# Optimization experiments

Measured on AMD Instinct MI355X. Metric: run time of the kernel, lower is better.

Reference implementation:

```python
import jax, jax.numpy as jnp
import numpy as np

TOP_K = 8
NUM_GROUPS = 8


def setup_inputs() -> dict:
    key = jax.random.key(0)
    ks = jax.random.split(key, 6)
    T_B, T_S, H, I, E, G = 1, 2048, 2048, 768, 32, NUM_GROUPS
    hidden_states = jax.random.normal(ks[0], (T_B, T_S, H), dtype=jnp.float32)
    gate_weight = jax.random.normal(ks[1], (E, H), dtype=jnp.float32) * 0.02
    gate_up_proj = jax.random.normal(ks[2], (E, 2 * I, H), dtype=jnp.float32) * 0.02
    down_proj = jax.random.normal(ks[3], (E, H, I), dtype=jnp.float32) * 0.02
    merge_groups = jax.random.randint(ks[4], (E,), 0, G, dtype=jnp.int64)
    # ensure every group id appears at least once so dominant experts are well-defined
    merge_groups = merge_groups.at[:G].set(jnp.arange(G, dtype=jnp.int64))
    dominant_experts = jax.random.randint(ks[5], (G,), 0, E, dtype=jnp.int64)
    return {
        "hidden_states": hidden_states,
        "gate_weight": gate_weight,
        "gate_up_proj": gate_up_proj,
        "down_proj": down_proj,
        "merge_groups": merge_groups,
        "dominant_experts": dominant_experts,
    }


def reference(hidden_states, gate_weight, gate_up_proj, down_proj, merge_groups, dominant_experts):
    B, S, H = hidden_states.shape
    G = dominant_experts.shape[0]
    x = hidden_states.reshape(-1, H)  # [T, H]

    # Router: softmax over all experts, then top-k of the probabilities (as in source)
    logits = jnp.einsum("th,eh->te", x, gate_weight)
    probs = jax.nn.softmax(logits.astype(jnp.float32), axis=-1).astype(logits.dtype)
    top_val, top_idx = jax.lax.top_k(probs, TOP_K)  # [T, K]
    top_val = top_val / jnp.sum(top_val, axis=-1, keepdims=True)  # norm_topk_prob

    # Each selected expert e is replaced by its group's dominant expert; by linearity
    # of the scatter-add combine, sum routing weights per (token, group).
    sel_group = merge_groups[top_idx]  # [T, K] in [0, G)
    onehot = jax.nn.one_hot(sel_group, G, dtype=top_val.dtype)  # [T, K, G]
    w_tg = jnp.einsum("tk,tkg->tg", top_val, onehot)  # combined weight per token/group

    gu = gate_up_proj[dominant_experts]  # [G, 2I, H]
    dn = down_proj[dominant_experts]     # [G, H, I]

    h = jnp.einsum("th,goh->tgo", x, gu)           # [T, G, 2I]
    gate, up = jnp.split(h, 2, axis=-1)              # [T, G, I] each
    act = jax.nn.silu(gate) * up                     # SwiGLU
    y = jnp.einsum("tgi,ghi->tgh", act, dn)        # [T, G, H]
    out = jnp.einsum("tg,tgh->th", w_tg, y)        # combine
    return out.reshape(B, S, H)
```

## Files before the change

kernel.cpp:

```cpp
#include <hip/hip_runtime.h>
#include <hip/hip_bf16.h>

typedef __attribute__((ext_vector_type(8))) short short8v;
typedef __attribute__((ext_vector_type(4))) float f32x4;

#define T_TOK 2048
#define HDIM  2048
#define IDIM  768
#define NGRP  8

__device__ __forceinline__ unsigned short f2b(float f){
  unsigned u = __float_as_uint(f);
  u = u + 0x7FFFu + ((u >> 16) & 1u);
  return (unsigned short)(u >> 16);
}
__device__ __forceinline__ float b2f(unsigned short s){
  return __uint_as_float(((unsigned)s) << 16);
}

__global__ __launch_bounds__(256) void router_kernel(
    const float* __restrict__ x, const float* __restrict__ gw,
    const int* __restrict__ mg, float* __restrict__ wtg,
    unsigned short* __restrict__ xb)
{
  __shared__ float xs[4][2048];
  __shared__ float lg[4][32];
  int tid = threadIdx.x;
  int t0 = blockIdx.x * 4;

  #pragma unroll
  for (int k = 0; k < 8; k++){
    int idx = k*256 + tid;
    int tok = idx >> 9, wi = idx & 511;
    float4 v = ((const float4*)(x + (size_t)(t0 + tok)*HDIM))[wi];
    ((float4*)xs[tok])[wi] = v;
    ushort4 b; b.x=f2b(v.x); b.y=f2b(v.y); b.z=f2b(v.z); b.w=f2b(v.w);
    ((ushort4*)(xb + (size_t)(t0+tok)*HDIM))[wi] = b;
  }
  __syncthreads();

  int e = tid >> 3, ch = tid & 7;
  float s0=0.f, s1=0.f, s2=0.f, s3=0.f;
  const float4* gv = (const float4*)(gw + (size_t)e*HDIM);
  #pragma unroll 4
  for (int k = 0; k < 64; k++){
    int i4 = ch + 8*k;
    float4 b  = gv[i4];
    float4 a0 = ((const float4*)xs[0])[i4];
    float4 a1 = ((const float4*)xs[1])[i4];
    float4 a2 = ((const float4*)xs[2])[i4];
    float4 a3 = ((const float4*)xs[3])[i4];
    s0 += a0.x*b.x + a0.y*b.y + a0.z*b.z + a0.w*b.w;
    s1 += a1.x*b.x + a1.y*b.y + a1.z*b.z + a1.w*b.w;
    s2 += a2.x*b.x + a2.y*b.y + a2.z*b.z + a2.w*b.w;
    s3 += a3.x*b.x + a3.y*b.y + a3.z*b.z + a3.w*b.w;
  }
  #pragma unroll
  for (int off=1; off<8; off<<=1){
    s0 += __shfl_xor(s0, off); s1 += __shfl_xor(s1, off);
    s2 += __shfl_xor(s2, off); s3 += __shfl_xor(s3, off);
  }
  if (ch == 0){ lg[0][e]=s0; lg[1][e]=s1; lg[2][e]=s2; lg[3][e]=s3; }
  __syncthreads();

  int wv = tid >> 6, lane = tid & 63;
  float val = (lane < 32) ? lg[wv][lane] : -1e30f;
  float mx = val;
  #pragma unroll
  for (int off=16; off; off>>=1) mx = fmaxf(mx, __shfl_xor(mx, off));
  float p = (lane < 32) ? expf(val - mx) : 0.f;
  float sm = p;
  #pragma unroll
  for (int off=16; off; off>>=1) sm += __shfl_xor(sm, off);
  float v = (lane < 32) ? (p / sm) : -1.f;
  int idx = lane;
  float vals[8]; int idxs[8];
  #pragma unroll
  for (int it=0; it<8; it++){
    float bv = v; int bi = idx;
    #pragma unroll
    for (int off=32; off; off>>=1){
      float ov = __shfl_xor(bv, off); int oi = __shfl_xor(bi, off);
      if (ov > bv || (ov == bv && oi < bi)){ bv = ov; bi = oi; }
    }
    vals[it] = bv; idxs[it] = bi;
    if (lane == bi) v = -1.f;
  }
  float tot = vals[0]+vals[1]+vals[2]+vals[3]+vals[4]+vals[5]+vals[6]+vals[7];
  float racc = 0.f;
  #pragma unroll
  for (int it=0; it<8; it++){
    int grp = mg[idxs[it]];
    if (lane == grp) racc += vals[it] / tot;
  }
  if (lane < 8) wtg[(size_t)(t0+wv)*NGRP + lane] = racc;
}

__global__ __launch_bounds__(256) void convert_gu_kernel(
    const float* __restrict__ src, unsigned short* __restrict__ dst,
    const int* __restrict__ de)
{
  int g = blockIdx.z;
  int i4 = blockIdx.x*256 + threadIdx.x;
  int j  = i4 >> 9;
  int c4 = i4 & 511;
  int q = j >> 5, r = j & 31;
  int srow = (r < 16) ? (q*16 + r) : (768 + q*16 + (r - 16));
  const float4* s = (const float4*)(src + ((size_t)de[g]*1536 + srow)*HDIM);
  float4 vv = s[c4];
  ushort4 b; b.x=f2b(vv.x); b.y=f2b(vv.y); b.z=f2b(vv.z); b.w=f2b(vv.w);
  ((ushort4*)(dst + ((size_t)g*1536 + j)*HDIM))[c4] = b;
}

__global__ __launch_bounds__(256) void convert_dn_kernel(
    const float* __restrict__ src, unsigned short* __restrict__ dst,
    const int* __restrict__ de)
{
  int g = blockIdx.z;
  size_t i4 = (size_t)blockIdx.x*256 + threadIdx.x;
  const float4* s = (const float4*)(src + (size_t)de[g]*1572864);
  float4 vv = s[i4];
  ushort4 b; b.x=f2b(vv.x); b.y=f2b(vv.y); b.z=f2b(vv.z); b.w=f2b(vv.w);
  ((ushort4*)(dst + (size_t)g*1572864))[i4] = b;
}


template<int R>
__device__ __forceinline__ void stage_tile(const unsigned short* __restrict__ gsrc,
                                           int ldE, unsigned short* __restrict__ lds,
                                           int tid)
{
  #pragma unroll
  for (int j = 0; j < R/128; j++){
    int row = j*128 + (tid >> 2);
    const unsigned short* src = gsrc + (size_t)row*ldE + (tid & 3)*8;
    __builtin_amdgcn_global_load_lds(
        (const __attribute__((address_space(1))) void*)src,
        (__attribute__((address_space(3))) void*)(lds + j*4096 + (tid >> 6)*512),
        16, 0, 0);
  }
}

__device__ __forceinline__ short8v rfrag(const unsigned short* lds, int r, int s){
  return *(const short8v*)((const char*)lds + r*64 + (s << 4));
}

#define WAITV(N)  asm volatile("s_waitcnt vmcnt(" #N ")" ::: "memory")
#define TOPBAR()  do { __builtin_amdgcn_s_barrier(); __builtin_amdgcn_sched_barrier(0); } while(0)

__global__ __launch_bounds__(512, 2) void gemm1_kernel(
    const unsigned short* __restrict__ xb, const unsigned short* __restrict__ gu,
    const float* __restrict__ wtg, unsigned short* __restrict__ actb)
{
  __shared__ unsigned short Al[4][8192];
  __shared__ unsigned short Bl[4][4096];
  int tid = threadIdx.x, lane = tid & 63, w = tid >> 6;
  int wm = w >> 1, wn = w & 1;
  int fr = lane & 15, sl = lane >> 4;

  int bid = blockIdx.x;
  int xcd = bid & 7, j = bid >> 3;
  int panel = ((xcd & 1) ? 48 : 0) + (j >> 1);
  int mb = ((xcd >> 1) << 1) + (j & 1);
  int nb = panel % 12, g = panel / 12;
  int m0 = mb * 256, n0 = nb * 128;
  const unsigned short* Abase = xb + (size_t)m0 * HDIM;
  const unsigned short* Bbase = gu + ((size_t)g * 1536 + n0) * HDIM;

  f32x4 acc[4][4];
  #pragma unroll
  for (int m=0;m<4;m++){
    #pragma unroll
    for (int n=0;n<4;n++) acc[m][n] = (f32x4){0,0,0,0};
  }

  #define BODY1(t, DOSTAGE) do { \
    int buf = (t) & 3; \
    short8v av[4], bv[4]; \
    _Pragma("unroll") for (int m=0;m<4;m++) av[m] = rfrag(&Al[buf][0], wm*64 + m*16 + fr, sl); \
    _Pragma("unroll") for (int n=0;n<4;n++) bv[n] = rfrag(&Bl[buf][0], wn*64 + n*16 + fr, sl); \
    if (DOSTAGE){ int k2 = (t)+3, b2 = k2 & 3; \
      stage_tile<256>(Abase + k2*32, HDIM, &Al[b2][0], tid); \
      stage_tile<128>(Bbase + k2*32, HDIM, &Bl[b2][0], tid); } \
    _Pragma("unroll") for (int m=0;m<4;m++){ \
      _Pragma("unroll") for (int n=0;n<4;n++){ \
        acc[m][n] = __builtin_amdgcn_mfma_f32_16x16x32_bf16(av[m], bv[n], acc[m][n],0,0,0); } } \
  } while(0)

  const int NT = 64;
  stage_tile<256>(Abase,      HDIM, &Al[0][0], tid); stage_tile<128>(Bbase,      HDIM, &Bl[0][0], tid);
  stage_tile<256>(Abase + 32, HDIM, &Al[1][0], tid); stage_tile<128>(Bbase + 32, HDIM, &Bl[1][0], tid);
  stage_tile<256>(Abase + 64, HDIM, &Al[2][0], tid); stage_tile<128>(Bbase + 64, HDIM, &Bl[2][0], tid);

  for (int t = 0; t < NT-3; ++t){
    WAITV(6); TOPBAR();
    BODY1(t, 1);
  }
  WAITV(6); TOPBAR(); BODY1(NT-3, 0);
  WAITV(3); TOPBAR(); BODY1(NT-2, 0);
  WAITV(0); TOPBAR(); BODY1(NT-1, 0);
  #undef BODY1

  int r0 = (lane >> 4) * 4;
  int q0 = (n0 + wn*64) >> 5;
  #pragma unroll
  for (int m = 0; m < 4; m++){
    int trow = m0 + wm*64 + m*16 + r0;
    #pragma unroll
    for (int q = 0; q < 2; q++){
      int icol = (q0 + q)*16 + fr;
      #pragma unroll
      for (int jj = 0; jj < 4; jj++){
        int t = trow + jj;
        float wv = wtg[(size_t)t*NGRP + g];
        float gf = acc[m][2*q][jj];
        float uf = acc[m][2*q+1][jj];
        float sg = gf / (1.f + expf(-gf));
        actb[((size_t)g*T_TOK + t)*IDIM + icol] = f2b(sg * uf * wv);
      }
    }
  }
}

__global__ __launch_bounds__(512, 2) void gemm2_kernel(
    const unsigned short* __restrict__ actb, const unsigned short* __restrict__ dnb,
    float* __restrict__ part)
{
  __shared__ unsigned short Al[4][4096];
  __shared__ unsigned short Bl[4][8192];
  int tid = threadIdx.x, lane = tid & 63, w = tid >> 6;
  int wm = w >> 2, wn = w & 3;
  int fr = lane & 15, sl = lane >> 4;

  int bid = blockIdx.x;
  int xcd = bid & 7, j = bid >> 3;
  int panel = ((xcd & 1) ? 8 : 0) + (j >> 2);
  int mb = ((xcd >> 1) << 2) + (j & 3);
  int nb = panel & 7, z = panel >> 3;
  int m0 = mb * 128, n0 = nb * 256;

  f32x4 acc[4][4];
  #pragma unroll
  for (int m=0;m<4;m++){
    #pragma unroll
    for (int n=0;n<4;n++) acc[m][n] = (f32x4){0,0,0,0};
  }

  #define STAGE2(kt, b2) do { \
    int gi = (kt) / 24; int kk = ((kt) - gi*24) * 32; int gg = z*4 + gi; \
    stage_tile<128>(actb + ((size_t)gg*T_TOK + m0)*IDIM + kk, IDIM, &Al[b2][0], tid); \
    stage_tile<256>(dnb  + ((size_t)gg*HDIM + n0)*IDIM + kk, IDIM, &Bl[b2][0], tid); \
  } while(0)

  #define BODY2(t, DOSTAGE) do { \
    int buf = (t) & 3; \
    short8v av[4], bv[4]; \
    _Pragma("unroll") for (int m=0;m<4;m++) av[m] = rfrag(&Al[buf][0], wm*64 + m*16 + fr, sl); \
    _Pragma("unroll") for (int n=0;n<4;n++) bv[n] = rfrag(&Bl[buf][0], wn*64 + n*16 + fr, sl); \
    if (DOSTAGE){ int k2 = (t)+3; STAGE2(k2, k2 & 3); } \
    _Pragma("unroll") for (int m=0;m<4;m++){ \
      _Pragma("unroll") for (int n=0;n<4;n++){ \
        acc[m][n] = __builtin_amdgcn_mfma_f32_16x16x32_bf16(av[m], bv[n], acc[m][n],0,0,0); } } \
  } while(0)

  const int NT = 96;
  STAGE2(0, 0); STAGE2(1, 1); STAGE2(2, 2);

  for (int t = 0; t < NT-3; ++t){
    WAITV(6); TOPBAR();
    BODY2(t, 1);
  }
  WAITV(6); TOPBAR(); BODY2(NT-3, 0);
  WAITV(3); TOPBAR(); BODY2(NT-2, 0);
  WAITV(0); TOPBAR(); BODY2(NT-1, 0);
  #undef BODY2
  #undef STAGE2

  float* Cb = part + (size_t)z * T_TOK * HDIM;
  int r0 = (lane >> 4) * 4;
  #pragma unroll
  for (int m = 0; m < 4; m++){
    int row = m0 + wm*64 + m*16 + r0;
    #pragma unroll
    for (int n = 0; n < 4; n++){
      int cc = n0 + wn*64 + n*16 + fr;
      #pragma unroll
      for (int jj = 0; jj < 4; jj++){
        Cb[(size_t)(row + jj)*HDIM + cc] = acc[m][n][jj];
      }
    }
  }
}

__global__ __launch_bounds__(256) void reduce_kernel(
    const float* __restrict__ p, float* __restrict__ o)
{
  size_t i = ((size_t)blockIdx.x*256 + threadIdx.x)*4;
  float4 a0 = *(const float4*)(p + i);
  float4 a1 = *(const float4*)(p + 4194304 + i);
  float4 r;
  r.x = a0.x + a1.x;
  r.y = a0.y + a1.y;
  r.z = a0.z + a1.z;
  r.w = a0.w + a1.w;
  *(float4*)(o + i) = r;
}

extern "C" void kernel_launch(void* const* d_in, const int* in_sizes, int n_in,
                              void* d_out, int out_size, void* d_ws, size_t ws_size,
                              hipStream_t stream)
{
  (void)in_sizes; (void)n_in; (void)out_size; (void)ws_size;
  const float* x   = (const float*)d_in[0];
  const float* gw  = (const float*)d_in[1];
  const float* gup = (const float*)d_in[2];
  const float* dnp = (const float*)d_in[3];
  const int*   mg  = (const int*)d_in[4];
  const int*   de  = (const int*)d_in[5];
  float* out = (float*)d_out;
  char* ws = (char*)d_ws;

  float*          wtg  = (float*)(ws + 0);
  unsigned short* xb   = (unsigned short*)(ws + 65536);
  unsigned short* dnb  = (unsigned short*)(ws + 8454144);
  unsigned short* actb = (unsigned short*)(ws + 33619968);
  unsigned short* gub  = (unsigned short*)(ws + 58785792);
  float*          part = (float*)(ws + 58785792);

  router_kernel<<<512, 256, 0, stream>>>(x, gw, mg, wtg, xb);
  convert_gu_kernel<<<dim3(3072,1,8), 256, 0, stream>>>(gup, gub, de);
  convert_dn_kernel<<<dim3(1536,1,8), 256, 0, stream>>>(dnp, dnb, de);
  gemm1_kernel<<<768, 512, 0, stream>>>(xb, gub, wtg, actb);
  gemm2_kernel<<<256, 512, 0, stream>>>(actb, dnb, part);
  reduce_kernel<<<4096, 256, 0, stream>>>(part, out);
}
```

Measured before the change: 253.9 us.

## Enlarge per-wave GEMM tiles, triple-buffer LDS, and split down-proj K four ways

gemm1 now runs 4 waves per block instead of 8, and each wave computes a 128x64 tile. This doubles MFMA work per LDS fragment load and shrinks the LDS ring to three stages with a prefetch distance of two. gemm2 moves to 256x256 tiles with K split four ways (two groups per split) instead of two, using the same triple-buffer scheme. Both GEMMs also wait on LDS reads before the MFMA block and raise wave priority around it. The reduce kernel now sums four fp32 partials, which adds extra global memory traffic, and the larger accumulator arrays raise register pressure.

```diff
diff --git a/kernel.cpp b/kernel.cpp
--- a/kernel.cpp
+++ b/kernel.cpp
@@ -126,9 +126,9 @@
 
 
 template<int R>
-__device__ __forceinline__ void stage_tile(const unsigned short* __restrict__ gsrc,
-                                           int ldE, unsigned short* __restrict__ lds,
-                                           int tid)
+__device__ __forceinline__ void stage512(const unsigned short* __restrict__ gsrc,
+                                         int ldE, unsigned short* __restrict__ lds,
+                                         int tid)
 {
   #pragma unroll
   for (int j = 0; j < R/128; j++){
@@ -141,19 +141,36 @@
   }
 }
 
+template<int R>
+__device__ __forceinline__ void stage256(const unsigned short* __restrict__ gsrc,
+                                         int ldE, unsigned short* __restrict__ lds,
+                                         int tid)
+{
+  #pragma unroll
+  for (int j = 0; j < R/64; j++){
+    int row = j*64 + (tid >> 2);
+    const unsigned short* src = gsrc + (size_t)row*ldE + (tid & 3)*8;
+    __builtin_amdgcn_global_load_lds(
+        (const __attribute__((address_space(1))) void*)src,
+        (__attribute__((address_space(3))) void*)(lds + j*2048 + (tid >> 6)*512),
+        16, 0, 0);
+  }
+}
+
 __device__ __forceinline__ short8v rfrag(const unsigned short* lds, int r, int s){
   return *(const short8v*)((const char*)lds + r*64 + (s << 4));
 }
 
 #define WAITV(N)  asm volatile("s_waitcnt vmcnt(" #N ")" ::: "memory")
 #define TOPBAR()  do { __builtin_amdgcn_s_barrier(); __builtin_amdgcn_sched_barrier(0); } while(0)
-
-__global__ __launch_bounds__(512, 2) void gemm1_kernel(
+#define PIN()     do { asm volatile("s_waitcnt lgkmcnt(0)" ::: "memory"); __builtin_amdgcn_sched_barrier(0); } while(0)
+
+__global__ __launch_bounds__(256, 2) void gemm1_kernel(
     const unsigned short* __restrict__ xb, const unsigned short* __restrict__ gu,
     const float* __restrict__ wtg, unsigned short* __restrict__ actb)
 {
-  __shared__ unsigned short Al[4][8192];
-  __shared__ unsigned short Bl[4][4096];
+  __shared__ unsigned short Al[3][8192];
+  __shared__ unsigned short Bl[3][4096];
   int tid = threadIdx.x, lane = tid & 63, w = tid >> 6;
   int wm = w >> 1, wn = w & 1;
   int fr = lane & 15, sl = lane >> 4;
@@ -167,45 +184,52 @@
   const unsigned short* Abase = xb + (size_t)m0 * HDIM;
   const unsigned short* Bbase = gu + ((size_t)g * 1536 + n0) * HDIM;
 
-  f32x4 acc[4][4];
-  #pragma unroll
-  for (int m=0;m<4;m++){
+  f32x4 acc[8][4];
+  #pragma unroll
+  for (int m=0;m<8;m++){
     #pragma unroll
     for (int n=0;n<4;n++) acc[m][n] = (f32x4){0,0,0,0};
   }
 
-  #define BODY1(t, DOSTAGE) do { \
-    int buf = (t) & 3; \
-    short8v av[4], bv[4]; \
-    _Pragma("unroll") for (int m=0;m<4;m++) av[m] = rfrag(&Al[buf][0], wm*64 + m*16 + fr, sl); \
-    _Pragma("unroll") for (int n=0;n<4;n++) bv[n] = rfrag(&Bl[buf][0], wn*64 + n*16 + fr, sl); \
-    if (DOSTAGE){ int k2 = (t)+3, b2 = k2 & 3; \
-      stage_tile<256>(Abase + k2*32, HDIM, &Al[b2][0], tid); \
-      stage_tile<128>(Bbase + k2*32, HDIM, &Bl[b2][0], tid); } \
-    _Pragma("unroll") for (int m=0;m<4;m++){ \
+  #define BODY1(t, CB, SB, DOSTAGE) do { \
+    const unsigned short* Ab = &Al[CB][0]; \
+    const unsigned short* Bb = &Bl[CB][0]; \
+    short8v av[8], bv[4]; \
+    _Pragma("unroll") for (int m=0;m<8;m++) av[m] = rfrag(Ab, wm*128 + m*16 + fr, sl); \
+    _Pragma("unroll") for (int n=0;n<4;n++) bv[n] = rfrag(Bb, wn*64 + n*16 + fr, sl); \
+    if (DOSTAGE){ int k2 = (t)+2; \
+      stage256<256>(Abase + k2*32, HDIM, &Al[SB][0], tid); \
+      stage256<128>(Bbase + k2*32, HDIM, &Bl[SB][0], tid); } \
+    PIN(); \
+    __builtin_amdgcn_s_setprio(1); \
+    _Pragma("unroll") for (int m=0;m<8;m++){ \
       _Pragma("unroll") for (int n=0;n<4;n++){ \
         acc[m][n] = __builtin_amdgcn_mfma_f32_16x16x32_bf16(av[m], bv[n], acc[m][n],0,0,0); } } \
+    __builtin_amdgcn_s_setprio(0); \
   } while(0)
 
   const int NT = 64;
-  stage_tile<256>(Abase,      HDIM, &Al[0][0], tid); stage_tile<128>(Bbase,      HDIM, &Bl[0][0], tid);
-  stage_tile<256>(Abase + 32, HDIM, &Al[1][0], tid); stage_tile<128>(Bbase + 32, HDIM, &Bl[1][0], tid);
-  stage_tile<256>(Abase + 64, HDIM, &Al[2][0], tid); stage_tile<128>(Bbase + 64, HDIM, &Bl[2][0], tid);
-
-  for (int t = 0; t < NT-3; ++t){
+  stage256<256>(Abase,      HDIM, &Al[0][0], tid);
+  stage256<128>(Bbase,      HDIM, &Bl[0][0], tid);
+  stage256<256>(Abase + 32, HDIM, &Al[1][0], tid);
+  stage256<128>(Bbase + 32, HDIM, &Bl[1][0], tid);
+
+  int cb = 0, sb = 2;
+  for (int t = 0; t < NT-2; ++t){
     WAITV(6); TOPBAR();
-    BODY1(t, 1);
-  }
-  WAITV(6); TOPBAR(); BODY1(NT-3, 0);
-  WAITV(3); TOPBAR(); BODY1(NT-2, 0);
-  WAITV(0); TOPBAR(); BODY1(NT-1, 0);
+    BODY1(t, cb, sb, 1);
+    cb = (cb==2)?0:cb+1; sb = (sb==2)?0:sb+1;
+  }
+  WAITV(6); TOPBAR(); BODY1(NT-2, cb, sb, 0);
+  cb = (cb==2)?0:cb+1;
+  WAITV(0); TOPBAR(); BODY1(NT-1, cb, sb, 0);
   #undef BODY1
 
   int r0 = (lane >> 4) * 4;
   int q0 = (n0 + wn*64) >> 5;
   #pragma unroll
-  for (int m = 0; m < 4; m++){
-    int trow = m0 + wm*64 + m*16 + r0;
+  for (int m = 0; m < 8; m++){
+    int trow = m0 + wm*128 + m*16 + r0;
     #pragma unroll
     for (int q = 0; q < 2; q++){
       int icol = (q0 + q)*16 + fr;
@@ -226,61 +250,67 @@
     const unsigned short* __restrict__ actb, const unsigned short* __restrict__ dnb,
     float* __restrict__ part)
 {
-  __shared__ unsigned short Al[4][4096];
-  __shared__ unsigned short Bl[4][8192];
+  __shared__ unsigned short Al[3][8192];
+  __shared__ unsigned short Bl[3][8192];
   int tid = threadIdx.x, lane = tid & 63, w = tid >> 6;
   int wm = w >> 2, wn = w & 3;
   int fr = lane & 15, sl = lane >> 4;
 
   int bid = blockIdx.x;
   int xcd = bid & 7, j = bid >> 3;
-  int panel = ((xcd & 1) ? 8 : 0) + (j >> 2);
-  int mb = ((xcd >> 1) << 2) + (j & 3);
+  int panel = ((xcd & 1) ? 16 : 0) + (j >> 1);
+  int mb = ((xcd >> 1) << 1) + (j & 1);
   int nb = panel & 7, z = panel >> 3;
-  int m0 = mb * 128, n0 = nb * 256;
-
-  f32x4 acc[4][4];
-  #pragma unroll
-  for (int m=0;m<4;m++){
+  int m0 = mb * 256, n0 = nb * 256;
+
+  f32x4 acc[8][4];
+  #pragma unroll
+  for (int m=0;m<8;m++){
     #pragma unroll
     for (int n=0;n<4;n++) acc[m][n] = (f32x4){0,0,0,0};
   }
 
-  #define STAGE2(kt, b2) do { \
-    int gi = (kt) / 24; int kk = ((kt) - gi*24) * 32; int gg = z*4 + gi; \
-    stage_tile<128>(actb + ((size_t)gg*T_TOK + m0)*IDIM + kk, IDIM, &Al[b2][0], tid); \
-    stage_tile<256>(dnb  + ((size_t)gg*HDIM + n0)*IDIM + kk, IDIM, &Bl[b2][0], tid); \
+  #define STAGE2(kt, SB) do { \
+    int gi = (kt) / 24; int kk = ((kt) - gi*24) * 32; int gg = z*2 + gi; \
+    stage512<256>(actb + ((size_t)gg*T_TOK + m0)*IDIM + kk, IDIM, &Al[SB][0], tid); \
+    stage512<256>(dnb  + ((size_t)gg*HDIM + n0)*IDIM + kk, IDIM, &Bl[SB][0], tid); \
   } while(0)
 
-  #define BODY2(t, DOSTAGE) do { \
-    int buf = (t) & 3; \
-    short8v av[4], bv[4]; \
-    _Pragma("unroll") for (int m=0;m<4;m++) av[m] = rfrag(&Al[buf][0], wm*64 + m*16 + fr, sl); \
-    _Pragma("unroll") for (int n=0;n<4;n++) bv[n] = rfrag(&Bl[buf][0], wn*64 + n*16 + fr, sl); \
-    if (DOSTAGE){ int k2 = (t)+3; STAGE2(k2, k2 & 3); } \
-    _Pragma("unroll") for (int m=0;m<4;m++){ \
+  #define BODY2(t, CB, SB, DOSTAGE) do { \
+    const unsigned short* Ab = &Al[CB][0]; \
+    const unsigned short* Bb = &Bl[CB][0]; \
+    short8v av[8], bv[4]; \
+    _Pragma("unroll") for (int m=0;m<8;m++) av[m] = rfrag(Ab, wm*128 + m*16 + fr, sl); \
+    _Pragma("unroll") for (int n=0;n<4;n++) bv[n] = rfrag(Bb, wn*64 + n*16 + fr, sl); \
+    if (DOSTAGE){ STAGE2((t)+2, SB); } \
+    PIN(); \
+    __builtin_amdgcn_s_setprio(1); \
+    _Pragma("unroll") for (int m=0;m<8;m++){ \
       _Pragma("unroll") for (int n=0;n<4;n++){ \
         acc[m][n] = __builtin_amdgcn_mfma_f32_16x16x32_bf16(av[m], bv[n], acc[m][n],0,0,0); } } \
+    __builtin_amdgcn_s_setprio(0); \
   } while(0)
 
-  const int NT = 96;
-  STAGE2(0, 0); STAGE2(1, 1); STAGE2(2, 2);
-
-  for (int t = 0; t < NT-3; ++t){
-    WAITV(6); TOPBAR();
-    BODY2(t, 1);
-  }
-  WAITV(6); TOPBAR(); BODY2(NT-3, 0);
-  WAITV(3); TOPBAR(); BODY2(NT-2, 0);
-  WAITV(0); TOPBAR(); BODY2(NT-1, 0);
+  const int NT = 48;
+  STAGE2(0, 0); STAGE2(1, 1);
+
+  int cb = 0, sb = 2;
+  for (int t = 0; t < NT-2; ++t){
+    WAITV(4); TOPBAR();
+    BODY2(t, cb, sb, 1);
+    cb = (cb==2)?0:cb+1; sb = (sb==2)?0:sb+1;
+  }
+  WAITV(4); TOPBAR(); BODY2(NT-2, cb, sb, 0);
+  cb = (cb==2)?0:cb+1;
+  WAITV(0); TOPBAR(); BODY2(NT-1, cb, sb, 0);
   #undef BODY2
   #undef STAGE2
 
   float* Cb = part + (size_t)z * T_TOK * HDIM;
   int r0 = (lane >> 4) * 4;
   #pragma unroll
-  for (int m = 0; m < 4; m++){
-    int row = m0 + wm*64 + m*16 + r0;
+  for (int m = 0; m < 8; m++){
+    int row = m0 + wm*128 + m*16 + r0;
     #pragma unroll
     for (int n = 0; n < 4; n++){
       int cc = n0 + wn*64 + n*16 + fr;
@@ -298,11 +328,13 @@
   size_t i = ((size_t)blockIdx.x*256 + threadIdx.x)*4;
   float4 a0 = *(const float4*)(p + i);
   float4 a1 = *(const float4*)(p + 4194304 + i);
+  float4 a2 = *(const float4*)(p + 8388608 + i);
+  float4 a3 = *(const float4*)(p + 12582912 + i);
   float4 r;
-  r.x = a0.x + a1.x;
-  r.y = a0.y + a1.y;
-  r.z = a0.z + a1.z;
-  r.w = a0.w + a1.w;
+  r.x = a0.x + a1.x + a2.x + a3.x;
+  r.y = a0.y + a1.y + a2.y + a3.y;
+  r.z = a0.z + a1.z + a2.z + a3.z;
+  r.w = a0.w + a1.w + a2.w + a3.w;
   *(float4*)(o + i) = r;
 }
 
@@ -330,7 +362,7 @@
   router_kernel<<<512, 256, 0, stream>>>(x, gw, mg, wtg, xb);
   convert_gu_kernel<<<dim3(3072,1,8), 256, 0, stream>>>(gup, gub, de);
   convert_dn_kernel<<<dim3(1536,1,8), 256, 0, stream>>>(dnp, dnb, de);
-  gemm1_kernel<<<768, 512, 0, stream>>>(xb, gub, wtg, actb);
+  gemm1_kernel<<<768, 256, 0, stream>>>(xb, gub, wtg, actb);
   gemm2_kernel<<<256, 512, 0, stream>>>(actb, dnb, part);
   reduce_kernel<<<4096, 256, 0, stream>>>(part, out);
 }
```

New measurement: 243.9 us. 1.04x faster.

## Restructure gemm1 to 4 waves with B fragments loaded directly to registers

Applied to the files above, without the earlier changes.

gemm1 drops from 512 to 256 threads per block. Each wave now covers 128 rows with an 8x4 accumulator tile, and the B operand is no longer staged through LDS but loaded straight into a triple-buffered register array. A 3-stage LDS ring for A replaces the 4-stage one. Both GEMMs also add an lgkmcnt wait plus a sched_barrier before the MFMA block and raise wave priority around it. The aim is to cut LDS traffic and shared memory use and raise MFMA density per wave, at the cost of much higher register pressure and less latency hiding on the direct global B loads.

```diff
diff --git a/kernel.cpp b/kernel.cpp
--- a/kernel.cpp
+++ b/kernel.cpp
@@ -126,9 +126,25 @@
 
 
 template<int R>
-__device__ __forceinline__ void stage_tile(const unsigned short* __restrict__ gsrc,
-                                           int ldE, unsigned short* __restrict__ lds,
-                                           int tid)
+__device__ __forceinline__ void stage256(const unsigned short* __restrict__ gsrc,
+                                         int ldE, unsigned short* __restrict__ lds,
+                                         int tid)
+{
+  #pragma unroll
+  for (int j = 0; j < R/64; j++){
+    int row = j*64 + (tid >> 2);
+    const unsigned short* src = gsrc + (size_t)row*ldE + (tid & 3)*8;
+    __builtin_amdgcn_global_load_lds(
+        (const __attribute__((address_space(1))) void*)src,
+        (__attribute__((address_space(3))) void*)(lds + j*2048 + (tid >> 6)*512),
+        16, 0, 0);
+  }
+}
+
+template<int R>
+__device__ __forceinline__ void stage512(const unsigned short* __restrict__ gsrc,
+                                         int ldE, unsigned short* __restrict__ lds,
+                                         int tid)
 {
   #pragma unroll
   for (int j = 0; j < R/128; j++){
@@ -147,13 +163,13 @@
 
 #define WAITV(N)  asm volatile("s_waitcnt vmcnt(" #N ")" ::: "memory")
 #define TOPBAR()  do { __builtin_amdgcn_s_barrier(); __builtin_amdgcn_sched_barrier(0); } while(0)
-
-__global__ __launch_bounds__(512, 2) void gemm1_kernel(
+#define PIN()     do { asm volatile("s_waitcnt lgkmcnt(0)" ::: "memory"); __builtin_amdgcn_sched_barrier(0); } while(0)
+
+__global__ __launch_bounds__(256, 2) void gemm1_kernel(
     const unsigned short* __restrict__ xb, const unsigned short* __restrict__ gu,
     const float* __restrict__ wtg, unsigned short* __restrict__ actb)
 {
-  __shared__ unsigned short Al[4][8192];
-  __shared__ unsigned short Bl[4][4096];
+  __shared__ unsigned short Al[3][8192];
   int tid = threadIdx.x, lane = tid & 63, w = tid >> 6;
   int wm = w >> 1, wn = w & 1;
   int fr = lane & 15, sl = lane >> 4;
@@ -165,47 +181,61 @@
   int nb = panel % 12, g = panel / 12;
   int m0 = mb * 256, n0 = nb * 128;
   const unsigned short* Abase = xb + (size_t)m0 * HDIM;
-  const unsigned short* Bbase = gu + ((size_t)g * 1536 + n0) * HDIM;
-
-  f32x4 acc[4][4];
-  #pragma unroll
-  for (int m=0;m<4;m++){
+
+  const unsigned short* Brow[4];
+  #pragma unroll
+  for (int n = 0; n < 4; n++)
+    Brow[n] = gu + ((size_t)g*1536 + n0 + wn*64 + n*16 + fr)*HDIM + sl*8;
+
+  f32x4 acc[8][4];
+  #pragma unroll
+  for (int m=0;m<8;m++){
     #pragma unroll
     for (int n=0;n<4;n++) acc[m][n] = (f32x4){0,0,0,0};
   }
-
-  #define BODY1(t, DOSTAGE) do { \
-    int buf = (t) & 3; \
-    short8v av[4], bv[4]; \
-    _Pragma("unroll") for (int m=0;m<4;m++) av[m] = rfrag(&Al[buf][0], wm*64 + m*16 + fr, sl); \
-    _Pragma("unroll") for (int n=0;n<4;n++) bv[n] = rfrag(&Bl[buf][0], wn*64 + n*16 + fr, sl); \
-    if (DOSTAGE){ int k2 = (t)+3, b2 = k2 & 3; \
-      stage_tile<256>(Abase + k2*32, HDIM, &Al[b2][0], tid); \
-      stage_tile<128>(Bbase + k2*32, HDIM, &Bl[b2][0], tid); } \
-    _Pragma("unroll") for (int m=0;m<4;m++){ \
+  short8v breg[3][4];
+
+  #define PFA(PT, PB)  stage256<256>(Abase + (PT)*32, HDIM, &Al[PB][0], tid)
+  #define PFB(PT, PB)  do { \
+    breg[PB][0] = *(const short8v*)(Brow[0] + (PT)*32); \
+    breg[PB][1] = *(const short8v*)(Brow[1] + (PT)*32); \
+    breg[PB][2] = *(const short8v*)(Brow[2] + (PT)*32); \
+    breg[PB][3] = *(const short8v*)(Brow[3] + (PT)*32); \
+  } while(0)
+
+  #define BODYA(t, CB, PT, PB, DOPF) do { \
+    short8v av[8]; \
+    _Pragma("unroll") for (int m=0;m<8;m++) av[m] = rfrag(&Al[CB][0], wm*128 + m*16 + fr, sl); \
+    if (DOPF){ PFA(PT, PB); PFB(PT, PB); } \
+    PIN(); \
+    __builtin_amdgcn_s_setprio(1); \
+    _Pragma("unroll") for (int m=0;m<8;m++){ \
       _Pragma("unroll") for (int n=0;n<4;n++){ \
-        acc[m][n] = __builtin_amdgcn_mfma_f32_16x16x32_bf16(av[m], bv[n], acc[m][n],0,0,0); } } \
+        acc[m][n] = __builtin_amdgcn_mfma_f32_16x16x32_bf16(av[m], breg[CB][n], acc[m][n],0,0,0); } } \
+    __builtin_amdgcn_s_setprio(0); \
   } while(0)
 
-  const int NT = 64;
-  stage_tile<256>(Abase,      HDIM, &Al[0][0], tid); stage_tile<128>(Bbase,      HDIM, &Bl[0][0], tid);
-  stage_tile<256>(Abase + 32, HDIM, &Al[1][0], tid); stage_tile<128>(Bbase + 32, HDIM, &Bl[1][0], tid);
-  stage_tile<256>(Abase + 64, HDIM, &Al[2][0], tid); stage_tile<128>(Bbase + 64, HDIM, &Bl[2][0], tid);
-
-  for (int t = 0; t < NT-3; ++t){
-    WAITV(6); TOPBAR();
-    BODY1(t, 1);
-  }
-  WAITV(6); TOPBAR(); BODY1(NT-3, 0);
-  WAITV(3); TOPBAR(); BODY1(NT-2, 0);
-  WAITV(0); TOPBAR(); BODY1(NT-1, 0);
-  #undef BODY1
+  PFA(0,0); PFB(0,0);
+  PFA(1,1); PFB(1,1);
+
+  for (int t = 0; t < 60; t += 3){
+    WAITV(8); TOPBAR(); BODYA(t  , 0, t+2, 2, 1);
+    WAITV(8); TOPBAR(); BODYA(t+1, 1, t+3, 0, 1);
+    WAITV(8); TOPBAR(); BODYA(t+2, 2, t+4, 1, 1);
+  }
+  WAITV(8); TOPBAR(); BODYA(60, 0, 62, 2, 1);
+  WAITV(8); TOPBAR(); BODYA(61, 1, 63, 0, 1);
+  WAITV(8); TOPBAR(); BODYA(62, 2, 0, 0, 0);
+  WAITV(0); TOPBAR(); BODYA(63, 0, 0, 0, 0);
+  #undef BODYA
+  #undef PFA
+  #undef PFB
 
   int r0 = (lane >> 4) * 4;
   int q0 = (n0 + wn*64) >> 5;
   #pragma unroll
-  for (int m = 0; m < 4; m++){
-    int trow = m0 + wm*64 + m*16 + r0;
+  for (int m = 0; m < 8; m++){
+    int trow = m0 + wm*128 + m*16 + r0;
     #pragma unroll
     for (int q = 0; q < 2; q++){
       int icol = (q0 + q)*16 + fr;
@@ -248,8 +278,8 @@
 
   #define STAGE2(kt, b2) do { \
     int gi = (kt) / 24; int kk = ((kt) - gi*24) * 32; int gg = z*4 + gi; \
-    stage_tile<128>(actb + ((size_t)gg*T_TOK + m0)*IDIM + kk, IDIM, &Al[b2][0], tid); \
-    stage_tile<256>(dnb  + ((size_t)gg*HDIM + n0)*IDIM + kk, IDIM, &Bl[b2][0], tid); \
+    stage512<128>(actb + ((size_t)gg*T_TOK + m0)*IDIM + kk, IDIM, &Al[b2][0], tid); \
+    stage512<256>(dnb  + ((size_t)gg*HDIM + n0)*IDIM + kk, IDIM, &Bl[b2][0], tid); \
   } while(0)
 
   #define BODY2(t, DOSTAGE) do { \
@@ -258,9 +288,12 @@
     _Pragma("unroll") for (int m=0;m<4;m++) av[m] = rfrag(&Al[buf][0], wm*64 + m*16 + fr, sl); \
     _Pragma("unroll") for (int n=0;n<4;n++) bv[n] = rfrag(&Bl[buf][0], wn*64 + n*16 + fr, sl); \
     if (DOSTAGE){ int k2 = (t)+3; STAGE2(k2, k2 & 3); } \
+    PIN(); \
+    __builtin_amdgcn_s_setprio(1); \
     _Pragma("unroll") for (int m=0;m<4;m++){ \
       _Pragma("unroll") for (int n=0;n<4;n++){ \
         acc[m][n] = __builtin_amdgcn_mfma_f32_16x16x32_bf16(av[m], bv[n], acc[m][n],0,0,0); } } \
+    __builtin_amdgcn_s_setprio(0); \
   } while(0)
 
   const int NT = 96;
@@ -330,7 +363,7 @@
   router_kernel<<<512, 256, 0, stream>>>(x, gw, mg, wtg, xb);
   convert_gu_kernel<<<dim3(3072,1,8), 256, 0, stream>>>(gup, gub, de);
   convert_dn_kernel<<<dim3(1536,1,8), 256, 0, stream>>>(dnp, dnb, de);
-  gemm1_kernel<<<768, 512, 0, stream>>>(xb, gub, wtg, actb);
+  gemm1_kernel<<<768, 256, 0, stream>>>(xb, gub, wtg, actb);
   gemm2_kernel<<<256, 512, 0, stream>>>(actb, dnb, part);
   reduce_kernel<<<4096, 256, 0, stream>>>(part, out);
 }
```

Measured after the change: 265.1 us. +4.4%, slower.

## Drop split-K in down GEMM, fuse weight conversions, add MFMA priority pinning

Applied to the files above, without the earlier changes.

The down-projection GEMM now runs the full K range (all 8 groups, 192 k-steps) in each block, using 128x128 tiles with 256 threads, and writes directly to the output. This removes the two partial buffers and the separate reduce kernel. The two weight-conversion kernels are merged into one launch, and both GEMMs wait on LDS reads and raise wave priority around the MFMA block. The trade-off is a longer serial K loop per block and smaller tiles that reuse less data in gemm2, while keeping the same 256-block grid.

```diff
diff --git a/kernel.cpp b/kernel.cpp
--- a/kernel.cpp
+++ b/kernel.cpp
@@ -96,39 +96,53 @@
   if (lane < 8) wtg[(size_t)(t0+wv)*NGRP + lane] = racc;
 }
 
-__global__ __launch_bounds__(256) void convert_gu_kernel(
-    const float* __restrict__ src, unsigned short* __restrict__ dst,
+__global__ __launch_bounds__(256) void convert_kernel(
+    const float* __restrict__ gup, const float* __restrict__ dnp,
+    unsigned short* __restrict__ gub, unsigned short* __restrict__ dnb,
     const int* __restrict__ de)
 {
   int g = blockIdx.z;
-  int i4 = blockIdx.x*256 + threadIdx.x;
-  int j  = i4 >> 9;
-  int c4 = i4 & 511;
-  int q = j >> 5, r = j & 31;
-  int srow = (r < 16) ? (q*16 + r) : (768 + q*16 + (r - 16));
-  const float4* s = (const float4*)(src + ((size_t)de[g]*1536 + srow)*HDIM);
-  float4 vv = s[c4];
-  ushort4 b; b.x=f2b(vv.x); b.y=f2b(vv.y); b.z=f2b(vv.z); b.w=f2b(vv.w);
-  ((ushort4*)(dst + ((size_t)g*1536 + j)*HDIM))[c4] = b;
-}
-
-__global__ __launch_bounds__(256) void convert_dn_kernel(
-    const float* __restrict__ src, unsigned short* __restrict__ dst,
-    const int* __restrict__ de)
-{
-  int g = blockIdx.z;
-  size_t i4 = (size_t)blockIdx.x*256 + threadIdx.x;
-  const float4* s = (const float4*)(src + (size_t)de[g]*1572864);
-  float4 vv = s[i4];
-  ushort4 b; b.x=f2b(vv.x); b.y=f2b(vv.y); b.z=f2b(vv.z); b.w=f2b(vv.w);
-  ((ushort4*)(dst + (size_t)g*1572864))[i4] = b;
+  int bx = blockIdx.x;
+  if (bx < 3072){
+    int i4 = bx*256 + threadIdx.x;
+    int j  = i4 >> 9;
+    int c4 = i4 & 511;
+    int q = j >> 5, r = j & 31;
+    int srow = (r < 16) ? (q*16 + r) : (768 + q*16 + (r - 16));
+    const float4* s = (const float4*)(gup + ((size_t)de[g]*1536 + srow)*HDIM);
+    float4 vv = s[c4];
+    ushort4 b; b.x=f2b(vv.x); b.y=f2b(vv.y); b.z=f2b(vv.z); b.w=f2b(vv.w);
+    ((ushort4*)(gub + ((size_t)g*1536 + j)*HDIM))[c4] = b;
+  } else {
+    size_t i4 = (size_t)(bx - 3072)*256 + threadIdx.x;
+    const float4* s = (const float4*)(dnp + (size_t)de[g]*1572864);
+    float4 vv = s[i4];
+    ushort4 b; b.x=f2b(vv.x); b.y=f2b(vv.y); b.z=f2b(vv.z); b.w=f2b(vv.w);
+    ((ushort4*)(dnb + (size_t)g*1572864))[i4] = b;
+  }
 }
 
 
 template<int R>
-__device__ __forceinline__ void stage_tile(const unsigned short* __restrict__ gsrc,
-                                           int ldE, unsigned short* __restrict__ lds,
-                                           int tid)
+__device__ __forceinline__ void stage256(const unsigned short* __restrict__ gsrc,
+                                         int ldE, unsigned short* __restrict__ lds,
+                                         int tid)
+{
+  #pragma unroll
+  for (int j = 0; j < R/64; j++){
+    int row = j*64 + (tid >> 2);
+    const unsigned short* src = gsrc + (size_t)row*ldE + (tid & 3)*8;
+    __builtin_amdgcn_global_load_lds(
+        (const __attribute__((address_space(1))) void*)src,
+        (__attribute__((address_space(3))) void*)(lds + j*2048 + (tid >> 6)*512),
+        16, 0, 0);
+  }
+}
+
+template<int R>
+__device__ __forceinline__ void stage512(const unsigned short* __restrict__ gsrc,
+                                         int ldE, unsigned short* __restrict__ lds,
+                                         int tid)
 {
   #pragma unroll
   for (int j = 0; j < R/128; j++){
@@ -147,6 +161,7 @@
 
 #define WAITV(N)  asm volatile("s_waitcnt vmcnt(" #N ")" ::: "memory")
 #define TOPBAR()  do { __builtin_amdgcn_s_barrier(); __builtin_amdgcn_sched_barrier(0); } while(0)
+#define PIN()     do { asm volatile("s_waitcnt lgkmcnt(0)" ::: "memory"); __builtin_amdgcn_sched_barrier(0); } while(0)
 
 __global__ __launch_bounds__(512, 2) void gemm1_kernel(
     const unsigned short* __restrict__ xb, const unsigned short* __restrict__ gu,
@@ -180,17 +195,20 @@
     _Pragma("unroll") for (int m=0;m<4;m++) av[m] = rfrag(&Al[buf][0], wm*64 + m*16 + fr, sl); \
     _Pragma("unroll") for (int n=0;n<4;n++) bv[n] = rfrag(&Bl[buf][0], wn*64 + n*16 + fr, sl); \
     if (DOSTAGE){ int k2 = (t)+3, b2 = k2 & 3; \
-      stage_tile<256>(Abase + k2*32, HDIM, &Al[b2][0], tid); \
-      stage_tile<128>(Bbase + k2*32, HDIM, &Bl[b2][0], tid); } \
+      stage512<256>(Abase + k2*32, HDIM, &Al[b2][0], tid); \
+      stage512<128>(Bbase + k2*32, HDIM, &Bl[b2][0], tid); } \
+    PIN(); \
+    __builtin_amdgcn_s_setprio(1); \
     _Pragma("unroll") for (int m=0;m<4;m++){ \
       _Pragma("unroll") for (int n=0;n<4;n++){ \
         acc[m][n] = __builtin_amdgcn_mfma_f32_16x16x32_bf16(av[m], bv[n], acc[m][n],0,0,0); } } \
+    __builtin_amdgcn_s_setprio(0); \
   } while(0)
 
   const int NT = 64;
-  stage_tile<256>(Abase,      HDIM, &Al[0][0], tid); stage_tile<128>(Bbase,      HDIM, &Bl[0][0], tid);
-  stage_tile<256>(Abase + 32, HDIM, &Al[1][0], tid); stage_tile<128>(Bbase + 32, HDIM, &Bl[1][0], tid);
-  stage_tile<256>(Abase + 64, HDIM, &Al[2][0], tid); stage_tile<128>(Bbase + 64, HDIM, &Bl[2][0], tid);
+  stage512<256>(Abase,      HDIM, &Al[0][0], tid); stage512<128>(Bbase,      HDIM, &Bl[0][0], tid);
+  stage512<256>(Abase + 32, HDIM, &Al[1][0], tid); stage512<128>(Bbase + 32, HDIM, &Bl[1][0], tid);
+  stage512<256>(Abase + 64, HDIM, &Al[2][0], tid); stage512<128>(Bbase + 64, HDIM, &Bl[2][0], tid);
 
   for (int t = 0; t < NT-3; ++t){
     WAITV(6); TOPBAR();
@@ -222,22 +240,21 @@
   }
 }
 
-__global__ __launch_bounds__(512, 2) void gemm2_kernel(
+__global__ __launch_bounds__(256, 2) void gemm2_kernel(
     const unsigned short* __restrict__ actb, const unsigned short* __restrict__ dnb,
-    float* __restrict__ part)
+    float* __restrict__ out)
 {
   __shared__ unsigned short Al[4][4096];
-  __shared__ unsigned short Bl[4][8192];
+  __shared__ unsigned short Bl[4][4096];
   int tid = threadIdx.x, lane = tid & 63, w = tid >> 6;
-  int wm = w >> 2, wn = w & 3;
+  int wm = w >> 1, wn = w & 1;
   int fr = lane & 15, sl = lane >> 4;
 
   int bid = blockIdx.x;
   int xcd = bid & 7, j = bid >> 3;
-  int panel = ((xcd & 1) ? 8 : 0) + (j >> 2);
-  int mb = ((xcd >> 1) << 2) + (j & 3);
-  int nb = panel & 7, z = panel >> 3;
-  int m0 = mb * 128, n0 = nb * 256;
+  int mb = (xcd << 1) | (j >> 4);
+  int nb = j & 15;
+  int m0 = mb * 128, n0 = nb * 128;
 
   f32x4 acc[4][4];
   #pragma unroll
@@ -247,9 +264,9 @@
   }
 
   #define STAGE2(kt, b2) do { \
-    int gi = (kt) / 24; int kk = ((kt) - gi*24) * 32; int gg = z*4 + gi; \
-    stage_tile<128>(actb + ((size_t)gg*T_TOK + m0)*IDIM + kk, IDIM, &Al[b2][0], tid); \
-    stage_tile<256>(dnb  + ((size_t)gg*HDIM + n0)*IDIM + kk, IDIM, &Bl[b2][0], tid); \
+    int gi = (kt) / 24; int kk = ((kt) - gi*24) * 32; \
+    stage256<128>(actb + ((size_t)(gi*T_TOK + m0))*IDIM + kk, IDIM, &Al[b2][0], tid); \
+    stage256<128>(dnb  + ((size_t)(gi*HDIM + n0))*IDIM + kk, IDIM, &Bl[b2][0], tid); \
   } while(0)
 
   #define BODY2(t, DOSTAGE) do { \
@@ -258,25 +275,27 @@
     _Pragma("unroll") for (int m=0;m<4;m++) av[m] = rfrag(&Al[buf][0], wm*64 + m*16 + fr, sl); \
     _Pragma("unroll") for (int n=0;n<4;n++) bv[n] = rfrag(&Bl[buf][0], wn*64 + n*16 + fr, sl); \
     if (DOSTAGE){ int k2 = (t)+3; STAGE2(k2, k2 & 3); } \
+    PIN(); \
+    __builtin_amdgcn_s_setprio(1); \
     _Pragma("unroll") for (int m=0;m<4;m++){ \
       _Pragma("unroll") for (int n=0;n<4;n++){ \
         acc[m][n] = __builtin_amdgcn_mfma_f32_16x16x32_bf16(av[m], bv[n], acc[m][n],0,0,0); } } \
+    __builtin_amdgcn_s_setprio(0); \
   } while(0)
 
-  const int NT = 96;
+  const int NT = 192;
   STAGE2(0, 0); STAGE2(1, 1); STAGE2(2, 2);
 
   for (int t = 0; t < NT-3; ++t){
-    WAITV(6); TOPBAR();
+    WAITV(8); TOPBAR();
     BODY2(t, 1);
   }
-  WAITV(6); TOPBAR(); BODY2(NT-3, 0);
-  WAITV(3); TOPBAR(); BODY2(NT-2, 0);
+  WAITV(8); TOPBAR(); BODY2(NT-3, 0);
+  WAITV(4); TOPBAR(); BODY2(NT-2, 0);
   WAITV(0); TOPBAR(); BODY2(NT-1, 0);
   #undef BODY2
   #undef STAGE2
 
-  float* Cb = part + (size_t)z * T_TOK * HDIM;
   int r0 = (lane >> 4) * 4;
   #pragma unroll
   for (int m = 0; m < 4; m++){
@@ -286,24 +305,10 @@
       int cc = n0 + wn*64 + n*16 + fr;
       #pragma unroll
       for (int jj = 0; jj < 4; jj++){
-        Cb[(size_t)(row + jj)*HDIM + cc] = acc[m][n][jj];
+        out[(size_t)(row + jj)*HDIM + cc] = acc[m][n][jj];
       }
     }
   }
-}
-
-__global__ __launch_bounds__(256) void reduce_kernel(
-    const float* __restrict__ p, float* __restrict__ o)
-{
-  size_t i = ((size_t)blockIdx.x*256 + threadIdx.x)*4;
-  float4 a0 = *(const float4*)(p + i);
-  float4 a1 = *(const float4*)(p + 4194304 + i);
-  float4 r;
-  r.x = a0.x + a1.x;
-  r.y = a0.y + a1.y;
-  r.z = a0.z + a1.z;
-  r.w = a0.w + a1.w;
-  *(float4*)(o + i) = r;
 }
 
 extern "C" void kernel_launch(void* const* d_in, const int* in_sizes, int n_in,
@@ -325,12 +330,9 @@
   unsigned short* dnb  = (unsigned short*)(ws + 8454144);
   unsigned short* actb = (unsigned short*)(ws + 33619968);
   unsigned short* gub  = (unsigned short*)(ws + 58785792);
-  float*          part = (float*)(ws + 58785792);
 
   router_kernel<<<512, 256, 0, stream>>>(x, gw, mg, wtg, xb);
-  convert_gu_kernel<<<dim3(3072,1,8), 256, 0, stream>>>(gup, gub, de);
-  convert_dn_kernel<<<dim3(1536,1,8), 256, 0, stream>>>(dnp, dnb, de);
+  convert_kernel<<<dim3(4608,1,8), 256, 0, stream>>>(gup, dnp, gub, dnb, de);
   gemm1_kernel<<<768, 512, 0, stream>>>(xb, gub, wtg, actb);
-  gemm2_kernel<<<256, 512, 0, stream>>>(actb, dnb, part);
-  reduce_kernel<<<4096, 256, 0, stream>>>(part, out);
-}
+  gemm2_kernel<<<256, 256, 0, stream>>>(actb, dnb, out);
+}
```

Measured after the change: 259.7 us. +2.3%, slower.
